# Performance work log

Hardware: AMD Instinct MI355X
Metric: run time of the kernel (lower is better)

The kernel has to match this reference:

```python
import jax, jax.numpy as jnp
import numpy as np

D_MODEL = 1024
N_HEADS = 16
D_K = D_MODEL // N_HEADS


def _glorot(key, fan_in, fan_out):
    limit = np.sqrt(6.0 / (fan_in + fan_out)).astype(np.float32)
    return jax.random.uniform(key, (fan_in, fan_out), jnp.float32, -limit, limit)


def setup_inputs() -> dict:
    key = jax.random.key(0)
    kx, kq, kk, kv = jax.random.split(key, 4)
    x = jax.random.normal(kx, (2, 2048, D_MODEL), jnp.float32)
    Wq = _glorot(kq, D_MODEL, D_MODEL)
    Wk = _glorot(kk, D_MODEL, D_MODEL)
    Wv = _glorot(kv, D_MODEL, D_MODEL)
    bq = jnp.zeros((D_MODEL,), jnp.float32)
    bk = jnp.zeros((D_MODEL,), jnp.float32)
    bv = jnp.zeros((D_MODEL,), jnp.float32)
    return {"x": x, "Wq": Wq, "bq": bq, "Wk": Wk, "bk": bk, "Wv": Wv, "bv": bv}


def reference(x, Wq, bq, Wk, bk, Wv, bv):
    B, S, _ = x.shape
    # QKV projections (Dense layers with bias)
    q = (x @ Wq + bq).reshape(B, S, N_HEADS, D_K).transpose(0, 2, 1, 3)  # [B,H,S,Dk]
    k = (x @ Wk + bk).reshape(B, S, N_HEADS, D_K).transpose(0, 2, 1, 3)
    v = (x @ Wv + bv).reshape(B, S, N_HEADS, D_K).transpose(0, 2, 1, 3)
    # raw exp-based softmax (NO max subtraction, per original module)
    scores = jnp.einsum('bhqd,bhkd->bhqk', q, k) / np.sqrt(D_K).astype(np.float32)
    scores = jnp.exp(scores)
    attn = scores / (jnp.sum(scores, axis=-1, keepdims=True) + 1e-8)
    context = jnp.einsum('bhqk,bhkd->bhqd', attn, v)  # [B,H,S,Dk]
    return context.transpose(0, 2, 1, 3).reshape(B, S, N_HEADS * D_K)
```

## Files before the change

### kernel.cpp

```cpp
#include <hip/hip_runtime.h>
#include <hip/hip_bf16.h>
#include <stdint.h>

typedef __bf16 bf16x8 __attribute__((ext_vector_type(8)));
typedef __bf16 bf16x4 __attribute__((ext_vector_type(4)));
typedef float  f32x4  __attribute__((ext_vector_type(4)));
typedef short  s16x4  __attribute__((ext_vector_type(4)));
typedef unsigned short u16_t;

#define MFMA(a, b, c)   __builtin_amdgcn_mfma_f32_16x16x32_bf16((a), (b), (c), 0, 0, 0)
#define MFMA16(a, b, c) __builtin_amdgcn_mfma_f32_16x16x16bf16_1k((a), (b), (c), 0, 0, 0)

__device__ __forceinline__ void cp16(const void* g, void* l) {
  __builtin_amdgcn_global_load_lds(
      (const __attribute__((address_space(1))) unsigned int*)g,
      (__attribute__((address_space(3))) unsigned int*)l, 16, 0, 0);
}

__global__ __launch_bounds__(256) void k_prep(const float* __restrict__ x,
                                              const float* __restrict__ W0,
                                              const float* __restrict__ W1,
                                              const float* __restrict__ W2,
                                              u16_t* __restrict__ xb,
                                              u16_t* __restrict__ Wt) {
  __shared__ u16_t T[64][65];
  int bx = blockIdx.x, t = threadIdx.x;
  if (bx < 4096) {
    int i = bx * 256 + t;
    float4 f = ((const float4*)x)[i];
    bf16x4 o = {(__bf16)f.x, (__bf16)f.y, (__bf16)f.z, (__bf16)f.w};
    *(bf16x4*)&xb[(size_t)i * 4] = o;
    return;
  }
  int j = bx - 4096;
  int nx = j & 15, ny = (j >> 4) & 15, z = j >> 8;
  const float* W = z == 0 ? W0 : (z == 1 ? W1 : W2);
  int k0 = ny * 64, n0 = nx * 64;
#pragma unroll
  for (int i = 0; i < 16; i++) {
    int e = i * 256 + t, r = e >> 6, c = e & 63;
    __bf16 hv = (__bf16)W[(size_t)(k0 + r) * 1024 + n0 + c];
    T[r][c] = *(u16_t*)&hv;
  }
  __syncthreads();
  size_t base = ((size_t)z * 1024 + n0) * 1024 + k0;
#pragma unroll
  for (int i = 0; i < 16; i++) {
    int e = i * 256 + t, r = e >> 6, c = e & 63;
    Wt[base + (size_t)r * 1024 + c] = T[c][r];
  }
}

__global__ __launch_bounds__(512, 2) void k_gemm_qkv(
    const u16_t* __restrict__ A, const u16_t* __restrict__ Bt,
    const float* __restrict__ bq, const float* __restrict__ bk,
    const float* __restrict__ bv,
    u16_t* __restrict__ Qo, u16_t* __restrict__ Ko, u16_t* __restrict__ Vo) {
  __shared__ u16_t smem[65536];
  u16_t* As = smem;
  u16_t* Bs = smem + 32768;

  const int tid = threadIdx.x, lane = tid & 63, wv = tid >> 6;
  const int quad = lane >> 4, col = lane & 15;
  const int wm = wv >> 2, wn = wv & 3;

  int bid = blockIdx.x;
  int wg = (bid & 7) * 24 + (bid >> 3);
  const int tn = (wg % 12) << 8, tm = (wg / 12) << 8;

  const int r16 = lane >> 2, c4 = lane & 3;
  const int srow = wv * 16 + r16;
  const int skoff = ((c4 ^ (r16 & 3)) << 3);
  const int sdst = srow * 32 + (c4 << 3);
  const size_t gA0 = (size_t)(tm + srow) * 1024 + skoff;
  const size_t gB0 = (size_t)(tn + srow) * 1024 + skoff;

  f32x4 acc[8][4] = {};

#define STAGE(kt, h, b) do {                                   \
    int d_ = (b) * 16384 + (h) * 8192 + sdst;                  \
    size_t s_ = (size_t)(kt) * 64 + (h) * 32;                  \
    cp16(A + gA0 + s_, As + d_);                               \
    cp16(A + gA0 + s_ + (size_t)128 * 1024, As + d_ + 4096);   \
    cp16(Bt + gB0 + s_, Bs + d_);                              \
    cp16(Bt + gB0 + s_ + (size_t)128 * 1024, Bs + d_ + 4096);  \
  } while (0)

#define BAR()    asm volatile("s_barrier" ::: "memory")
#define WAITV(N) asm volatile("s_waitcnt vmcnt(" #N ")" ::: "memory")
#define WAITL()  asm volatile("s_waitcnt lgkmcnt(0)" ::: "memory")
#define SCHED0() __builtin_amdgcn_sched_barrier(0)

  STAGE(0, 0, 0);
  STAGE(0, 1, 0);
  WAITV(4);
  BAR();

  const int swz8 = (((lane >> 4) ^ (col & 3)) << 3);
  const int abase = (wm * 128 + col) * 32 + swz8;
  const int bbase = (wn * 64 + col) * 32 + swz8;

  for (int t = 0; t < 16; ++t) {
    const int cur = t & 1, nxt = cur ^ 1;
    const u16_t* Ap = As + cur * 16384;
    const u16_t* Bp = Bs + cur * 16384;
    bf16x8 af[4], bf[4];

#pragma unroll
    for (int i = 0; i < 4; i++) af[i] = *(const bf16x8*)&Ap[abase + i * 512];
#pragma unroll
    for (int i = 0; i < 4; i++) bf[i] = *(const bf16x8*)&Bp[bbase + i * 512];
    if (t + 1 < 16) STAGE(t + 1, 0, nxt);
    BAR(); WAITL(); SCHED0();
    __builtin_amdgcn_s_setprio(1);
#pragma unroll
    for (int i = 0; i < 4; i++)
#pragma unroll
      for (int j = 0; j < 4; j++) acc[i][j] = MFMA(af[i], bf[j], acc[i][j]);
    __builtin_amdgcn_s_setprio(0);
    BAR();

#pragma unroll
    for (int i = 0; i < 4; i++) af[i] = *(const bf16x8*)&Ap[abase + (i + 4) * 512];
    if (t + 1 < 16) { STAGE(t + 1, 1, nxt); WAITV(8); }
    else            { WAITV(0); }
    BAR(); WAITL(); SCHED0();
    __builtin_amdgcn_s_setprio(1);
#pragma unroll
    for (int i = 0; i < 4; i++)
#pragma unroll
      for (int j = 0; j < 4; j++) acc[i + 4][j] = MFMA(af[i], bf[j], acc[i + 4][j]);
    __builtin_amdgcn_s_setprio(0);
    BAR();

#pragma unroll
    for (int i = 0; i < 4; i++) af[i] = *(const bf16x8*)&Ap[8192 + abase + i * 512];
#pragma unroll
    for (int i = 0; i < 4; i++) bf[i] = *(const bf16x8*)&Bp[8192 + bbase + i * 512];
    BAR(); WAITL(); SCHED0();
    __builtin_amdgcn_s_setprio(1);
#pragma unroll
    for (int i = 0; i < 4; i++)
#pragma unroll
      for (int j = 0; j < 4; j++) acc[i][j] = MFMA(af[i], bf[j], acc[i][j]);
    __builtin_amdgcn_s_setprio(0);
    BAR();

#pragma unroll
    for (int i = 0; i < 4; i++) af[i] = *(const bf16x8*)&Ap[8192 + abase + (i + 4) * 512];
    if (t + 1 < 16) WAITV(4);
    WAITL();
    BAR(); SCHED0();
    __builtin_amdgcn_s_setprio(1);
#pragma unroll
    for (int i = 0; i < 4; i++)
#pragma unroll
      for (int j = 0; j < 4; j++) acc[i + 4][j] = MFMA(af[i], bf[j], acc[i + 4][j]);
    __builtin_amdgcn_s_setprio(0);
    BAR();
  }

#undef STAGE

  const int mat = tn >> 10;
  const float* bias = mat == 0 ? bq : (mat == 1 ? bk : bv);
  if (mat == 2) {
#pragma unroll
    for (int nt = 0; nt < 4; nt++) {
      int gn = tn + wn * 64 + nt * 16 + col;
      int d = gn & 1023, h = d >> 6, dk = d & 63;
      float bb = bias[d];
#pragma unroll
      for (int mt = 0; mt < 8; mt++) {
        int gm = tm + wm * 128 + mt * 16 + quad * 4;
        int b = gm >> 11, s = gm & 2047;
        bf16x4 pk4;
#pragma unroll
        for (int r = 0; r < 4; r++) pk4[r] = (__bf16)(acc[mt][nt][r] + bb);
        *(bf16x4*)&Vo[((size_t)((b * 16 + h) * 64 + dk)) * 2048 + s] = pk4;
      }
    }
  } else {
    u16_t* O = mat == 0 ? Qo : Ko;
    const float scl = mat == 0 ? 0.18033688011112042f : 1.0f;
#pragma unroll
    for (int nt = 0; nt < 4; nt++) {
      int gn = tn + wn * 64 + nt * 16 + col;
      int d = gn & 1023, h = d >> 6, dk = d & 63;
      float bb = bias[d];
#pragma unroll
      for (int mt = 0; mt < 8; mt++) {
#pragma unroll
        for (int r = 0; r < 4; r++) {
          int gm = tm + wm * 128 + mt * 16 + quad * 4 + r;
          int b = gm >> 11, s = gm & 2047;
          __bf16 hv = (__bf16)((acc[mt][nt][r] + bb) * scl);
          O[((size_t)((b * 16 + h) * 2048 + s)) * 64 + dk] = *(u16_t*)&hv;
        }
      }
    }
  }
}

__global__ __launch_bounds__(256, 4) void k_attn(const u16_t* __restrict__ Q,
                                                 const u16_t* __restrict__ K,
                                                 const u16_t* __restrict__ Vt,
                                                 float* __restrict__ out) {
  __shared__ u16_t smem[20480];
  u16_t* Qs  = smem;
  u16_t* Ksb = smem + 4096;
  u16_t* Vsb = smem + 12288;
  const int tid = threadIdx.x, lane = tid & 63, wv = tid >> 6;
  const int quad = lane >> 4, col = lane & 15;
  const int qh = wv >> 1, kh = wv & 1;

  const int bid = blockIdx.x;
  const int bh = (bid & 7) + 8 * ((bid >> 3) >> 5);
  const int qt = (bid >> 3) & 31;
  const int b = bh >> 4, h = bh & 15;
  const int r8 = lane >> 3, c8 = lane & 7;

  const u16_t* Qg = Q + ((size_t)bh * 2048 + qt * 64) * 64;
  const u16_t* Kg = K + (size_t)bh * 2048 * 64;
  const u16_t* Vg = Vt + (size_t)bh * 64 * 2048;

#pragma unroll
  for (int i = 0; i < 2; i++) {
    int c = wv * 2 + i;
    int row = c * 8 + r8;
    int lch = c8 ^ r8;
    cp16(Qg + (size_t)row * 64 + lch * 8, Qs + c * 512 + lane * 8);
    cp16(Kg + (size_t)row * 64 + lch * 8, Ksb + c * 512 + lane * 8);
    cp16(Vg + (size_t)row * 2048 + lch * 8, Vsb + c * 512 + lane * 8);
  }
  __syncthreads();

  bf16x8 qf[2][2];
#pragma unroll
  for (int nt = 0; nt < 2; nt++)
#pragma unroll
    for (int ks = 0; ks < 2; ks++) {
      int row = qh * 32 + nt * 16 + col;
      qf[nt][ks] = *(const bf16x8*)&Qs[row * 64 + (((ks * 4 + quad) ^ (row & 7)) * 8)];
    }

  const short one_bf = (short)0x3F80;
  s16x4 ones4 = {one_bf, one_bf, one_bf, one_bf};

  f32x4 ao[2][4] = {};
  f32x4 dn[2] = {};

#pragma unroll 2
  for (int kt = 0; kt < 32; kt++) {
    const int cur = kt & 1;
    const u16_t* Kc = Ksb + cur * 4096;
    const u16_t* Vc = Vsb + cur * 4096;
    if (kt + 1 < 32) {
      u16_t* Kn = Ksb + (cur ^ 1) * 4096;
      u16_t* Vn = Vsb + (cur ^ 1) * 4096;
#pragma unroll
      for (int i = 0; i < 2; i++) {
        int c = wv * 2 + i;
        int row = c * 8 + r8;
        int lch = c8 ^ r8;
        cp16(Kg + (size_t)(kt + 1) * 4096 + (size_t)row * 64 + lch * 8,
             Kn + c * 512 + lane * 8);
        cp16(Vg + (size_t)row * 2048 + (kt + 1) * 64 + lch * 8,
             Vn + c * 512 + lane * 8);
      }
    }

    f32x4 sc[2][2] = {};
#pragma unroll
    for (int ks = 0; ks < 2; ks++) {
      bf16x8 kf[2];
#pragma unroll
      for (int mt = 0; mt < 2; mt++) {
        int row = kh * 32 + mt * 16 + col;
        kf[mt] = *(const bf16x8*)&Kc[row * 64 + (((ks * 4 + quad) ^ (row & 7)) * 8)];
      }
#pragma unroll
      for (int mt = 0; mt < 2; mt++)
#pragma unroll
        for (int nt = 0; nt < 2; nt++)
          sc[mt][nt] = MFMA(kf[mt], qf[nt][ks], sc[mt][nt]);
    }

    s16x4 pf[2][2];
#pragma unroll
    for (int mt = 0; mt < 2; mt++)
#pragma unroll
      for (int nt = 0; nt < 2; nt++) {
#pragma unroll
        for (int r = 0; r < 4; r++) {
          __bf16 e = (__bf16)__builtin_amdgcn_exp2f(sc[mt][nt][r]);
          pf[mt][nt][r] = *(short*)&e;
        }
        dn[nt] = MFMA16(pf[mt][nt], ones4, dn[nt]);
      }

#pragma unroll
    for (int mt = 0; mt < 2; mt++) {
#pragma unroll
      for (int dt = 0; dt < 4; dt++) {
        int row = dt * 16 + col;
        int c = kh * 4 + mt * 2 + (quad >> 1);
        int addr = row * 64 + ((c ^ (row & 7)) * 8) + (quad & 1) * 4;
        s16x4 vf = *(const s16x4*)&Vc[addr];
#pragma unroll
        for (int nt = 0; nt < 2; nt++)
          ao[nt][dt] = MFMA16(pf[mt][nt], vf, ao[nt][dt]);
      }
    }
    __syncthreads();
  }

  float* red = (float*)(smem + 4096);
  const int rb = (qh * 64 + lane) * 41;
  if (kh == 1) {
#pragma unroll
    for (int nt = 0; nt < 2; nt++) {
#pragma unroll
      for (int dt = 0; dt < 4; dt++)
#pragma unroll
        for (int r = 0; r < 4; r++)
          red[rb + (nt * 4 + dt) * 4 + r] = ao[nt][dt][r];
#pragma unroll
      for (int r = 0; r < 4; r++)
        red[rb + 32 + nt * 4 + r] = dn[nt][r];
    }
  }
  __syncthreads();
  if (kh == 0) {
#pragma unroll
    for (int nt = 0; nt < 2; nt++) {
      float dsum[4];
#pragma unroll
      for (int r = 0; r < 4; r++)
        dsum[r] = dn[nt][r] + red[rb + 32 + nt * 4 + r] + 1e-8f;
#pragma unroll
      for (int dt = 0; dt < 4; dt++) {
#pragma unroll
        for (int r = 0; r < 4; r++) {
          float v = (ao[nt][dt][r] + red[rb + (nt * 4 + dt) * 4 + r]) / dsum[r];
          int s = qt * 64 + qh * 32 + nt * 16 + quad * 4 + r;
          out[((size_t)b * 2048 + s) * 1024 + h * 64 + dt * 16 + col] = v;
        }
      }
    }
  }
}

extern "C" void kernel_launch(void* const* d_in, const int* in_sizes, int n_in,
                              void* d_out, int out_size, void* d_ws, size_t ws_size,
                              hipStream_t stream) {
  const float* x  = (const float*)d_in[0];
  const float* Wq = (const float*)d_in[1];
  const float* bq = (const float*)d_in[2];
  const float* Wk = (const float*)d_in[3];
  const float* bk = (const float*)d_in[4];
  const float* Wv = (const float*)d_in[5];
  const float* bv = (const float*)d_in[6];
  float* out = (float*)d_out;

  char* ws = (char*)d_ws;
  u16_t* xb  = (u16_t*)(ws);
  u16_t* Wt  = (u16_t*)(ws + 8388608);
  u16_t* Qb  = (u16_t*)(ws + 14680064);
  u16_t* Kb  = (u16_t*)(ws + 23068672);
  u16_t* Vtb = (u16_t*)(ws + 31457280);

  hipLaunchKernelGGL(k_prep, dim3(4864), dim3(256), 0, stream, x, Wq, Wk, Wv, xb, Wt);
  hipLaunchKernelGGL(k_gemm_qkv, dim3(192), dim3(512), 0, stream,
                     xb, Wt, bq, bk, bv, Qb, Kb, Vtb);
  hipLaunchKernelGGL(k_attn, dim3(1024), dim3(256), 0, stream, Qb, Kb, Vtb, out);
}
```

Before: 174.7 us.

## Software-pipeline attention loop: overlap PV of previous tile with QK of current

Restructures the attention inner loop so the P·V MFMAs for the previous key tile run alongside the QK^T MFMAs of the current tile, while the exp conversion for the current tile follows. V loads now lag K by one tile, using double-buffered P fragments and a separate epilogue for the final PV step. It also raises wave priority around the MFMA section and replaces per-element division with a reciprocal multiply in the output normalization. The gain depends on hiding exp/VALU latency behind matrix work, at the cost of more live registers.

```diff
diff --git a/kernel.cpp b/kernel.cpp
--- a/kernel.cpp
+++ b/kernel.cpp
@@ -231,7 +231,6 @@
     int lch = c8 ^ r8;
     cp16(Qg + (size_t)row * 64 + lch * 8, Qs + c * 512 + lane * 8);
     cp16(Kg + (size_t)row * 64 + lch * 8, Ksb + c * 512 + lane * 8);
-    cp16(Vg + (size_t)row * 2048 + lch * 8, Vsb + c * 512 + lane * 8);
   }
   __syncthreads();
 
@@ -249,56 +248,80 @@
 
   f32x4 ao[2][4] = {};
   f32x4 dn[2] = {};
-
-#pragma unroll 2
-  for (int kt = 0; kt < 32; kt++) {
-    const int cur = kt & 1;
-    const u16_t* Kc = Ksb + cur * 4096;
-    const u16_t* Vc = Vsb + cur * 4096;
-    if (kt + 1 < 32) {
-      u16_t* Kn = Ksb + (cur ^ 1) * 4096;
-      u16_t* Vn = Vsb + (cur ^ 1) * 4096;
-#pragma unroll
-      for (int i = 0; i < 2; i++) {
-        int c = wv * 2 + i;
-        int row = c * 8 + r8;
-        int lch = c8 ^ r8;
-        cp16(Kg + (size_t)(kt + 1) * 4096 + (size_t)row * 64 + lch * 8,
-             Kn + c * 512 + lane * 8);
-        cp16(Vg + (size_t)row * 2048 + (kt + 1) * 64 + lch * 8,
-             Vn + c * 512 + lane * 8);
-      }
-    }
-
-    f32x4 sc[2][2] = {};
-#pragma unroll
-    for (int ks = 0; ks < 2; ks++) {
-      bf16x8 kf[2];
-#pragma unroll
-      for (int mt = 0; mt < 2; mt++) {
-        int row = kh * 32 + mt * 16 + col;
-        kf[mt] = *(const bf16x8*)&Kc[row * 64 + (((ks * 4 + quad) ^ (row & 7)) * 8)];
-      }
-#pragma unroll
-      for (int mt = 0; mt < 2; mt++)
-#pragma unroll
-        for (int nt = 0; nt < 2; nt++)
-          sc[mt][nt] = MFMA(kf[mt], qf[nt][ks], sc[mt][nt]);
-    }
-
-    s16x4 pf[2][2];
-#pragma unroll
-    for (int mt = 0; mt < 2; mt++)
-#pragma unroll
-      for (int nt = 0; nt < 2; nt++) {
-#pragma unroll
-        for (int r = 0; r < 4; r++) {
-          __bf16 e = (__bf16)__builtin_amdgcn_exp2f(sc[mt][nt][r]);
-          pf[mt][nt][r] = *(short*)&e;
-        }
-        dn[nt] = MFMA16(pf[mt][nt], ones4, dn[nt]);
-      }
-
+  s16x4 pfA[2][2] = {}, pfB[2][2] = {};
+
+#define ATTN_STEP(KT, CUR, PFW, PFR, DO_PV) do {                                      \
+    const u16_t* Kc = Ksb + (CUR) * 4096;                                             \
+    const u16_t* Vp = Vsb + ((CUR) ^ 1) * 4096;                                       \
+    u16_t* Kn = Ksb + ((CUR) ^ 1) * 4096;                                             \
+    u16_t* Vn = Vsb + (CUR) * 4096;                                                   \
+    _Pragma("unroll")                                                                 \
+    for (int i = 0; i < 2; i++) {                                                     \
+      int c = wv * 2 + i;                                                             \
+      int row = c * 8 + r8;                                                           \
+      int lch = c8 ^ r8;                                                              \
+      if ((KT) + 1 < 32)                                                              \
+        cp16(Kg + (size_t)((KT) + 1) * 4096 + (size_t)row * 64 + lch * 8,             \
+             Kn + c * 512 + lane * 8);                                                \
+      cp16(Vg + (size_t)row * 2048 + (KT) * 64 + lch * 8,                             \
+           Vn + c * 512 + lane * 8);                                                  \
+    }                                                                                 \
+    f32x4 sc[2][2] = {};                                                              \
+    __builtin_amdgcn_s_setprio(1);                                                    \
+    _Pragma("unroll")                                                                 \
+    for (int ks = 0; ks < 2; ks++) {                                                  \
+      bf16x8 kf[2];                                                                   \
+      _Pragma("unroll")                                                               \
+      for (int mt = 0; mt < 2; mt++) {                                                \
+        int row = kh * 32 + mt * 16 + col;                                            \
+        kf[mt] = *(const bf16x8*)&Kc[row * 64 + (((ks * 4 + quad) ^ (row & 7)) * 8)]; \
+      }                                                                               \
+      _Pragma("unroll")                                                               \
+      for (int mt = 0; mt < 2; mt++)                                                  \
+        _Pragma("unroll")                                                             \
+        for (int nt = 0; nt < 2; nt++)                                                \
+          sc[mt][nt] = MFMA(kf[mt], qf[nt][ks], sc[mt][nt]);                          \
+    }                                                                                 \
+    if (DO_PV) {                                                                      \
+      _Pragma("unroll")                                                               \
+      for (int mt = 0; mt < 2; mt++) {                                                \
+        _Pragma("unroll")                                                             \
+        for (int dt = 0; dt < 4; dt++) {                                              \
+          int row = dt * 16 + col;                                                    \
+          int c = kh * 4 + mt * 2 + (quad >> 1);                                      \
+          int addr = row * 64 + ((c ^ (row & 7)) * 8) + (quad & 1) * 4;               \
+          s16x4 vf = *(const s16x4*)&Vp[addr];                                        \
+          _Pragma("unroll")                                                           \
+          for (int nt = 0; nt < 2; nt++)                                              \
+            ao[nt][dt] = MFMA16(PFR[mt][nt], vf, ao[nt][dt]);                         \
+        }                                                                             \
+      }                                                                               \
+    }                                                                                 \
+    __builtin_amdgcn_s_setprio(0);                                                    \
+    _Pragma("unroll")                                                                 \
+    for (int mt = 0; mt < 2; mt++)                                                    \
+      _Pragma("unroll")                                                               \
+      for (int nt = 0; nt < 2; nt++) {                                                \
+        _Pragma("unroll")                                                             \
+        for (int r = 0; r < 4; r++) {                                                 \
+          __bf16 e = (__bf16)__builtin_amdgcn_exp2f(sc[mt][nt][r]);                   \
+          PFW[mt][nt][r] = *(short*)&e;                                               \
+        }                                                                             \
+        dn[nt] = MFMA16(PFW[mt][nt], ones4, dn[nt]);                                  \
+      }                                                                               \
+    __syncthreads();                                                                  \
+  } while (0)
+
+#pragma unroll 1
+  for (int kt2 = 0; kt2 < 16; kt2++) {
+    int kt0 = kt2 * 2;
+    ATTN_STEP(kt0,     0, pfA, pfB, (kt0 > 0));
+    ATTN_STEP(kt0 + 1, 1, pfB, pfA, 1);
+  }
+#undef ATTN_STEP
+
+  {
+    const u16_t* Vp = Vsb + 4096;
 #pragma unroll
     for (int mt = 0; mt < 2; mt++) {
 #pragma unroll
@@ -306,13 +329,12 @@
         int row = dt * 16 + col;
         int c = kh * 4 + mt * 2 + (quad >> 1);
         int addr = row * 64 + ((c ^ (row & 7)) * 8) + (quad & 1) * 4;
-        s16x4 vf = *(const s16x4*)&Vc[addr];
+        s16x4 vf = *(const s16x4*)&Vp[addr];
 #pragma unroll
         for (int nt = 0; nt < 2; nt++)
-          ao[nt][dt] = MFMA16(pf[mt][nt], vf, ao[nt][dt]);
+          ao[nt][dt] = MFMA16(pfB[mt][nt], vf, ao[nt][dt]);
       }
     }
-    __syncthreads();
   }
 
   float* red = (float*)(smem + 4096);
@@ -334,15 +356,15 @@
   if (kh == 0) {
 #pragma unroll
     for (int nt = 0; nt < 2; nt++) {
-      float dsum[4];
+      float inv[4];
 #pragma unroll
       for (int r = 0; r < 4; r++)
-        dsum[r] = dn[nt][r] + red[rb + 32 + nt * 4 + r] + 1e-8f;
+        inv[r] = 1.0f / (dn[nt][r] + red[rb + 32 + nt * 4 + r] + 1e-8f);
 #pragma unroll
       for (int dt = 0; dt < 4; dt++) {
 #pragma unroll
         for (int r = 0; r < 4; r++) {
-          float v = (ao[nt][dt][r] + red[rb + (nt * 4 + dt) * 4 + r]) / dsum[r];
+          float v = (ao[nt][dt][r] + red[rb + (nt * 4 + dt) * 4 + r]) * inv[r];
           int s = qt * 64 + qh * 32 + nt * 16 + quad * 4 + r;
           out[((size_t)b * 2048 + s) * 1024 + h * 64 + dt * 16 + col] = v;
         }
```

Result: no change. 174.9 us (+0.1%).
